# Kernel tuning notes

Measured on AMD Instinct MI355X. Metric: run time of the kernel, lower is better.

The kernel has to match this reference:

```python
import jax, jax.numpy as jnp
import numpy as np
from jax import lax

K = 3            # exact neighbors per node in setup -> inner loop bound
MAX_STEPS = K + 1  # each step removes a candidate; sentinel ends the loop


def setup_inputs() -> dict:
    key = jax.random.key(0)
    ks = jax.random.split(key, 10)
    N, Fin, E, H1, H2 = 128, 512, 128, 256, 128
    nbrs = jax.random.randint(ks[0], (N, K), 0, N)
    adj = jnp.zeros((N, N), jnp.float32).at[jnp.arange(N)[:, None], nbrs].set(1.0)
    feature_origin = jax.random.normal(ks[1], (N, Fin), jnp.float32)
    labels = jax.random.randint(ks[2], (N,), 0, 7)

    def lin(k, fi, fo):
        return (jax.random.normal(k, (fi, fo), jnp.float32) / np.float32(np.sqrt(fi)))

    return {
        "adj": adj, "feature_origin": feature_origin, "labels": labels,
        "W_e": lin(ks[3], Fin, E), "b_e": jnp.zeros((E,), jnp.float32),
        "W1": lin(ks[4], 2 * E, H1), "b1": jnp.zeros((H1,), jnp.float32),
        "W2": lin(ks[5], H1, H2), "b2": jnp.zeros((H2,), jnp.float32),
        "w_lk": lin(ks[6], H2, 1), "b_lk": jnp.zeros((1,), jnp.float32),
        "w_act": lin(ks[7], H2, 2), "b_act": jnp.zeros((2,), jnp.float32),
    }


def _forward(adj, feature_origin, W_e, b_e, W1, b1, W2, b2, w_lk, b_lk, w_act, b_act):
    N = feature_origin.shape[0]
    E = W_e.shape[1]
    embed = lambda x: jax.nn.relu(x @ W_e + b_e)
    mlp = lambda s: jax.nn.relu(jax.nn.relu(s @ W1 + b1) @ W2 + b2)
    feature0 = embed(feature_origin)                      # [N, E]
    # original quirk: `if v > 0` -> node 0 (and sentinel) get a zero neighbor feature
    nonzero_row = (jnp.arange(N) > 0)[:, None]

    def node_fn(carry, i):
        feature, updated = carry
        cand = adj[i] != 0                                # remaining candidate mask
        sel = jnp.zeros((N,), bool)                       # signal_neighbor_i as mask

        def step_fn(st, _):
            feature, cand, sel, updated, done = st
            x_i = feature[i]
            nbr = jnp.where(nonzero_row, feature, 0.0)
            s = jnp.concatenate([jnp.broadcast_to(x_i, (N, E)), nbr], axis=-1)
            sentinel = jnp.concatenate([x_i, jnp.zeros_like(x_i)])[None]
            s = jnp.concatenate([s, sentinel], axis=0)    # [N+1, 2E]
            hidden = mlp(s)                               # [N+1, H2]
            lk = (hidden @ w_lk + b_lk)[:, 0]             # [N+1]
            valid = jnp.concatenate([cand, jnp.ones((1,), bool)])
            # deterministic surrogate for Categorical sampling: argmax of dist
            ut = jnp.argmax(jnp.where(valid, lk, -jnp.inf))
            is_end = ut == N
            skip = done | is_end
            utc = jnp.minimum(ut, N - 1)
            at = (jnp.argmax(hidden[utc] @ w_act + b_act) == 1).astype(feature.dtype)
            x_ut = feature_origin[utc]
            x_self = feature_origin[i]
            self_f = sel.astype(feature.dtype)
            cnt = self_f.sum()
            sel_sum = self_f @ feature_origin
            hv = (sel_sum + at * x_ut + x_self) / (cnt + at + 1.0)
            feat2 = feature.at[i].set(embed(hv)).at[utc].set(embed(x_ut))
            feature = jnp.where(skip, feature, feat2)
            upd2 = updated.at[i].set(True).at[utc].set(True)
            updated = jnp.where(skip, updated, upd2)
            sel = sel.at[utc].set(jnp.where(skip, sel[utc], (at == 1.0) | sel[utc]))
            cand = cand.at[utc].set(jnp.where(skip, cand[utc], False))
            return (feature, cand, sel, updated, skip), None

        (feature, _, _, updated, _), _ = lax.scan(
            step_fn, (feature, cand, sel, updated, jnp.array(False)),
            None, length=MAX_STEPS)
        return (feature, updated), None

    (feature, updated), _ = lax.scan(
        node_fn, (feature0, jnp.zeros((N,), bool)), jnp.arange(N))
    # embedding mirrors every write to feature; untouched rows stay zero
    return jnp.where(updated[:, None], feature, 0.0)


def reference(adj, feature_origin, labels, W_e, b_e, W1, b1, W2, b2, w_lk, b_lk, w_act, b_act):
    return _forward(adj, feature_origin, W_e, b_e, W1, b1, W2, b2,
                    w_lk, b_lk, w_act, b_act)
```

## Files before the change

kernel.cpp:

```cpp
#include <hip/hip_runtime.h>
#include <math.h>

constexpr int Nn  = 128;
constexpr int FIN = 512;
constexpr int EE  = 128;
constexpr int H1n = 256;
constexpr int H2n = 128;

__global__ void precomp1(const float* __restrict__ fo, const float* __restrict__ We,
                         const float* __restrict__ be,
                         float* __restrict__ G0, float* __restrict__ feat)
{
    const int n = blockIdx.x;
    const int j = threadIdx.x;
    float acc = 0.f;
    for (int k = 0; k < FIN; ++k)
        acc += fo[n * FIN + k] * We[k * EE + j];
    G0[n * EE + j] = acc;
    feat[n * EE + j] = fmaxf(acc + be[j], 0.f);
}

__global__ void precomp2(const float* __restrict__ G0, const float* __restrict__ be,
                         const float* __restrict__ W1,
                         float* __restrict__ Bcur, float* __restrict__ B0)
{
    __shared__ float f[EE];
    const int n = blockIdx.x;
    const int j = threadIdx.x;
    if (j < EE) f[j] = fmaxf(G0[n * EE + j] + be[j], 0.f);
    __syncthreads();
    float acc = 0.f;
    for (int k = 0; k < EE; ++k)
        acc += f[k] * W1[(EE + k) * H1n + j];
    Bcur[n * H1n + j] = acc;
    if (B0) B0[n * H1n + j] = acc;
}

__global__ __launch_bounds__(512, 2) void seqk(
    const float* __restrict__ adj,  const float* __restrict__ W1,
    const float* __restrict__ b1,   const float* __restrict__ W2,
    const float* __restrict__ b2,   const float* __restrict__ wlk,
    const float* __restrict__ blkb, const float* __restrict__ wact,
    const float* __restrict__ bact, const float* __restrict__ be,
    const float* __restrict__ G0,   const float* __restrict__ B0,
    float* __restrict__ feat,       float* __restrict__ Bcur)
{
    __shared__ float w2t[H2n * H1n];
    __shared__ float x[EE];
    __shared__ float u[H1n];
    __shared__ float ubi[H1n];
    __shared__ float h1[4][H1n];
    __shared__ float h2[4][H2n];
    __shared__ float pa[4][4][H2n];
    __shared__ float gsum[EE], rowf[EE], sbe[EE];
    __shared__ float sb1[H1n], sb2[H2n], swlk[H2n], swact[2 * H2n];
    __shared__ float rb_lk[8], rb_a0[8], rb_a1[8];
    __shared__ float sblk, sba0, sba1;
    __shared__ int   candlist[4];
    __shared__ unsigned long long cand_mask[2], sel_mask[2], upd_mask[2];
    __shared__ int   ncand_s, ut_s, at_s, brk_s, rr_s, needb_s, xdirty_s;
    __shared__ float cnt_s;

    const int tid = threadIdx.x;

    float w1reg[128];
    {
        const int col = tid & 255;
        const int rbase = (tid < 256) ? 0 : EE;
        #pragma unroll
        for (int k = 0; k < 128; ++k)
            w1reg[k] = W1[(rbase + k) * H1n + col];
    }
    for (int idx = tid; idx < H1n * H2n; idx += 512) {
        const int k = idx >> 7, j = idx & 127;
        const int cg = k >> 2, w = k & 3;
        w2t[j * H1n + (((cg ^ (j & 7)) << 2) | w)] = W2[k * H2n + j];
    }
    if (tid < EE)  sbe[tid] = be[tid];
    if (tid < H1n) sb1[tid] = b1[tid];
    if (tid < H2n) { sb2[tid] = b2[tid]; swlk[tid] = wlk[tid]; }
    if (tid < 2 * H2n) swact[tid] = wact[tid];
    if (tid == 0) { sblk = blkb[0]; sba0 = bact[0]; sba1 = bact[1]; }
    if (tid < 2) upd_mask[tid] = 0ULL;
    __syncthreads();

    for (int i = 0; i < Nn; ++i) {
        if (tid < EE) { gsum[tid] = 0.f; x[tid] = feat[i * EE + tid]; }
        if (tid == 0) { cnt_s = 0.f; sel_mask[0] = 0ULL; sel_mask[1] = 0ULL; xdirty_s = 0; }
        if (tid < Nn) {
            const bool c = adj[i * Nn + tid] != 0.f;
            const unsigned long long m = __ballot(c);
            if ((tid & 63) == 0) cand_mask[tid >> 6] = m;
        }
        __syncthreads();
        if (tid == 0) {
            int nc = 0, selfc = 0;
            for (int w = 0; w < 2; ++w) {
                unsigned long long m = cand_mask[w];
                while (m && nc < 4) {
                    const int b = __builtin_ctzll(m);
                    const int v = w * 64 + b;
                    candlist[nc++] = v;
                    if (v == i) selfc = 1;
                    m &= m - 1;
                }
            }
            ncand_s = nc; needb_s = selfc;
        }
        __syncthreads();

        for (int s = 0; s < 4; ++s) {
            if (tid < 256 || needb_s) {
                float a0 = 0.f, a1 = 0.f, a2 = 0.f, a3 = 0.f;
                #pragma unroll
                for (int q = 0; q < 32; ++q) {
                    const float4 xv = *reinterpret_cast<const float4*>(&x[q * 4]);
                    a0 += xv.x * w1reg[q * 4 + 0];
                    a1 += xv.y * w1reg[q * 4 + 1];
                    a2 += xv.z * w1reg[q * 4 + 2];
                    a3 += xv.w * w1reg[q * 4 + 3];
                }
                const float sres = (a0 + a1) + (a2 + a3);
                if (tid < 256) u[tid] = sres; else ubi[tid - 256] = sres;
            }
            __syncthreads();

            {
                const int nrows = ncand_s + 1;
                #pragma unroll
                for (int hh = 0; hh < 2; ++hh) {
                    const int idx = hh * 512 + tid;
                    const int r = idx >> 8, k = idx & 255;
                    float hv = 0.f;
                    if (r < nrows) {
                        const int v = (r < ncand_s) ? candlist[r] : -1;
                        float Bv = 0.f;
                        if (v > 0) Bv = (v == i && needb_s) ? ubi[k] : Bcur[v * H1n + k];
                        hv = fmaxf(u[k] + Bv + sb1[k], 0.f);
                    }
                    h1[r][k] = hv;
                }
            }
            __syncthreads();

            {
                const int kq = tid >> 7, j = tid & 127;
                const int sw = j & 7;
                float ac0 = 0.f, ac1 = 0.f, ac2 = 0.f, ac3 = 0.f;
                #pragma unroll
                for (int kk = 0; kk < 16; ++kk) {
                    const int cg = kq * 16 + kk;
                    const float4 wv = *reinterpret_cast<const float4*>(
                        &w2t[j * H1n + ((cg ^ sw) << 2)]);
                    const int k0 = cg << 2;
                    const float4 h0 = *reinterpret_cast<const float4*>(&h1[0][k0]);
                    const float4 h1v = *reinterpret_cast<const float4*>(&h1[1][k0]);
                    const float4 h2v = *reinterpret_cast<const float4*>(&h1[2][k0]);
                    const float4 h3v = *reinterpret_cast<const float4*>(&h1[3][k0]);
                    ac0 += h0.x * wv.x + h0.y * wv.y + h0.z * wv.z + h0.w * wv.w;
                    ac1 += h1v.x * wv.x + h1v.y * wv.y + h1v.z * wv.z + h1v.w * wv.w;
                    ac2 += h2v.x * wv.x + h2v.y * wv.y + h2v.z * wv.z + h2v.w * wv.w;
                    ac3 += h3v.x * wv.x + h3v.y * wv.y + h3v.z * wv.z + h3v.w * wv.w;
                }
                pa[kq][0][j] = ac0; pa[kq][1][j] = ac1;
                pa[kq][2][j] = ac2; pa[kq][3][j] = ac3;
            }
            __syncthreads();

            {
                const int r = tid >> 7, j = tid & 127;
                const float v = pa[0][r][j] + pa[1][r][j] + pa[2][r][j] + pa[3][r][j]
                                + sb2[j];
                const float hval = fmaxf(v, 0.f);
                h2[r][j] = hval;
                float plk = hval * swlk[j];
                float p0  = hval * swact[2 * j];
                float p1  = hval * swact[2 * j + 1];
                #pragma unroll
                for (int off = 32; off; off >>= 1) {
                    plk += __shfl_down(plk, off);
                    p0  += __shfl_down(p0, off);
                    p1  += __shfl_down(p1, off);
                }
                if ((tid & 63) == 0) {
                    const int w = tid >> 6;
                    rb_lk[w] = plk; rb_a0[w] = p0; rb_a1[w] = p1;
                }
            }
            __syncthreads();

            if (tid == 0) {
                float lkv[4];
                #pragma unroll
                for (int r = 0; r < 4; ++r) lkv[r] = rb_lk[2 * r] + rb_lk[2 * r + 1] + sblk;
                float bv = -INFINITY; int ut = -1, rsel = -1;
                for (int r2 = 0; r2 < ncand_s; ++r2)
                    if (lkv[r2] > bv) { bv = lkv[r2]; ut = candlist[r2]; rsel = r2; }
                if (ut < 0 || lkv[ncand_s] > bv) ut = Nn;
                ut_s = ut;
                brk_s = (ut == Nn);
                if (!brk_s) {
                    rr_s = rsel;
                    const float a0 = rb_a0[2 * rsel] + rb_a0[2 * rsel + 1] + sba0;
                    const float a1 = rb_a1[2 * rsel] + rb_a1[2 * rsel + 1] + sba1;
                    at_s = (a1 > a0) ? 1 : 0;
                }
            }
            __syncthreads();
            if (brk_s) break;

            {
                const int utc = ut_s;
                const float at = (float)at_s;
                const bool selOld = (sel_mask[utc >> 6] >> (utc & 63)) & 1ULL;
                const float denom = cnt_s + at + 1.0f;
                if (tid < EE) {
                    const float g_ut = G0[utc * EE + tid];
                    const float futc = fmaxf(g_ut + sbe[tid], 0.f);
                    const float z = (gsum[tid] + at * g_ut + G0[i * EE + tid]) / denom
                                    + sbe[tid];
                    float nx = fmaxf(z, 0.f);
                    if (utc == i) nx = futc;
                    x[tid] = nx;
                    if (utc != i) feat[i * EE + tid] = nx;
                    feat[utc * EE + tid] = futc;
                    rowf[tid] = futc;
                    if (at_s && !selOld) gsum[tid] += g_ut;
                }
                if (B0 != nullptr && tid < H1n)
                    Bcur[utc * H1n + tid] = B0[utc * H1n + tid];
            }
            __syncthreads();

            if (tid == 0) {
                const int utc = ut_s;
                const bool selOld = (sel_mask[utc >> 6] >> (utc & 63)) & 1ULL;
                if (at_s && !selOld) { cnt_s += 1.f; sel_mask[utc >> 6] |= (1ULL << (utc & 63)); }
                cand_mask[utc >> 6] &= ~(1ULL << (utc & 63));
                upd_mask[i >> 6]   |= (1ULL << (i & 63));
                upd_mask[utc >> 6] |= (1ULL << (utc & 63));
                xdirty_s = (utc != i) ? 1 : 0;
                int nc = 0, selfc = 0;
                for (int w = 0; w < 2; ++w) {
                    unsigned long long m = cand_mask[w];
                    while (m && nc < 4) {
                        const int b = __builtin_ctzll(m);
                        const int v = w * 64 + b;
                        candlist[nc++] = v;
                        if (v == i) selfc = 1;
                        m &= m - 1;
                    }
                }
                ncand_s = nc; needb_s = selfc;
            }
            if (B0 == nullptr && tid >= 256) {
                float a0 = 0.f, a1 = 0.f, a2 = 0.f, a3 = 0.f;
                #pragma unroll
                for (int q = 0; q < 32; ++q) {
                    const float4 xv = *reinterpret_cast<const float4*>(&rowf[q * 4]);
                    a0 += xv.x * w1reg[q * 4 + 0];
                    a1 += xv.y * w1reg[q * 4 + 1];
                    a2 += xv.z * w1reg[q * 4 + 2];
                    a3 += xv.w * w1reg[q * 4 + 3];
                }
                Bcur[ut_s * H1n + (tid - 256)] = (a0 + a1) + (a2 + a3);
            }
            __syncthreads();
        }

        if (xdirty_s && tid >= 256) {
            float a0 = 0.f, a1 = 0.f, a2 = 0.f, a3 = 0.f;
            #pragma unroll
            for (int q = 0; q < 32; ++q) {
                const float4 xv = *reinterpret_cast<const float4*>(&x[q * 4]);
                a0 += xv.x * w1reg[q * 4 + 0];
                a1 += xv.y * w1reg[q * 4 + 1];
                a2 += xv.z * w1reg[q * 4 + 2];
                a3 += xv.w * w1reg[q * 4 + 3];
            }
            Bcur[i * H1n + (tid - 256)] = (a0 + a1) + (a2 + a3);
        }
        __syncthreads();
    }

    for (int idx = tid; idx < Nn * EE; idx += 512) {
        const int n = idx >> 7;
        const float v = feat[idx];
        feat[idx] = ((upd_mask[n >> 6] >> (n & 63)) & 1ULL) ? v : 0.f;
    }
}

extern "C" void kernel_launch(void* const* d_in, const int* in_sizes, int n_in,
                              void* d_out, int out_size, void* d_ws, size_t ws_size,
                              hipStream_t stream)
{
    (void)in_sizes; (void)n_in; (void)out_size;
    const float* adj  = (const float*)d_in[0];
    const float* fo   = (const float*)d_in[1];
    const float* We   = (const float*)d_in[3];
    const float* be   = (const float*)d_in[4];
    const float* W1   = (const float*)d_in[5];
    const float* b1   = (const float*)d_in[6];
    const float* W2   = (const float*)d_in[7];
    const float* b2   = (const float*)d_in[8];
    const float* wlk  = (const float*)d_in[9];
    const float* blkb = (const float*)d_in[10];
    const float* wact = (const float*)d_in[11];
    const float* bact = (const float*)d_in[12];

    float* ws   = (float*)d_ws;
    float* G0   = ws;
    float* Bcur = ws + 16384;
    float* B0   = (ws_size >= (size_t)(64 + 128 + 128) * 1024) ? (ws + 49152) : nullptr;
    float* feat = (float*)d_out;

    hipLaunchKernelGGL(precomp1, dim3(Nn), dim3(EE), 0, stream, fo, We, be, G0, feat);
    hipLaunchKernelGGL(precomp2, dim3(Nn), dim3(H1n), 0, stream, G0, be, W1, Bcur, B0);
    hipLaunchKernelGGL(seqk, dim3(1), dim3(512), 0, stream,
                       adj, W1, b1, W2, b2, wlk, blkb, wact, bact, be,
                       G0, B0, feat, Bcur);
}
```

Measured before the change: 1.970 ms.

## Move per-step control to registers, keep Bcur in LDS and W2 in registers

Result: slower. 2.285 ms (+16.0%).

```diff
diff --git a/kernel.cpp b/kernel.cpp
--- a/kernel.cpp
+++ b/kernel.cpp
@@ -22,7 +22,7 @@
 
 __global__ void precomp2(const float* __restrict__ G0, const float* __restrict__ be,
                          const float* __restrict__ W1,
-                         float* __restrict__ Bcur, float* __restrict__ B0)
+                         float* __restrict__ BcurG)
 {
     __shared__ float f[EE];
     const int n = blockIdx.x;
@@ -32,8 +32,7 @@
     float acc = 0.f;
     for (int k = 0; k < EE; ++k)
         acc += f[k] * W1[(EE + k) * H1n + j];
-    Bcur[n * H1n + j] = acc;
-    if (B0) B0[n * H1n + j] = acc;
+    BcurG[n * H1n + j] = acc;
 }
 
 __global__ __launch_bounds__(512, 2) void seqk(
@@ -42,24 +41,19 @@
     const float* __restrict__ b2,   const float* __restrict__ wlk,
     const float* __restrict__ blkb, const float* __restrict__ wact,
     const float* __restrict__ bact, const float* __restrict__ be,
-    const float* __restrict__ G0,   const float* __restrict__ B0,
-    float* __restrict__ feat,       float* __restrict__ Bcur)
+    const float* __restrict__ G0,   const float* __restrict__ BcurG,
+    float* __restrict__ feat)
 {
-    __shared__ float w2t[H2n * H1n];
-    __shared__ float x[EE];
+    __shared__ float bc[Nn * H1n];
+    __shared__ float h1[4][H1n];
+    __shared__ float pa[4][4][H2n];
     __shared__ float u[H1n];
     __shared__ float ubi[H1n];
-    __shared__ float h1[4][H1n];
-    __shared__ float h2[4][H2n];
-    __shared__ float pa[4][4][H2n];
-    __shared__ float gsum[EE], rowf[EE], sbe[EE];
-    __shared__ float sb1[H1n], sb2[H2n], swlk[H2n], swact[2 * H2n];
+    __shared__ float xsh[EE], gi[EE], gsum[EE];
+    __shared__ float gc[3 * EE];
+    __shared__ float sbe[EE], sb1[H1n], sb2[H2n], swlk[H2n], swact[2 * H2n];
     __shared__ float rb_lk[8], rb_a0[8], rb_a1[8];
-    __shared__ float sblk, sba0, sba1;
-    __shared__ int   candlist[4];
-    __shared__ unsigned long long cand_mask[2], sel_mask[2], upd_mask[2];
-    __shared__ int   ncand_s, ut_s, at_s, brk_s, rr_s, needb_s, xdirty_s;
-    __shared__ float cnt_s;
+    __shared__ unsigned long long mlds[2];
 
     const int tid = threadIdx.x;
 
@@ -71,50 +65,70 @@
         for (int k = 0; k < 128; ++k)
             w1reg[k] = W1[(rbase + k) * H1n + col];
     }
-    for (int idx = tid; idx < H1n * H2n; idx += 512) {
-        const int k = idx >> 7, j = idx & 127;
-        const int cg = k >> 2, w = k & 3;
-        w2t[j * H1n + (((cg ^ (j & 7)) << 2) | w)] = W2[k * H2n + j];
+    float w2reg[64];
+    {
+        const int kq = tid >> 7, j = tid & 127;
+        #pragma unroll
+        for (int kk = 0; kk < 64; ++kk)
+            w2reg[kk] = W2[(kq * 64 + kk) * H2n + j];
+    }
+    #pragma unroll
+    for (int q = 0; q < 16; ++q) {
+        const int idx = (q * 512 + tid) * 4;
+        *reinterpret_cast<float4*>(&bc[idx]) =
+            *reinterpret_cast<const float4*>(&BcurG[idx]);
     }
     if (tid < EE)  sbe[tid] = be[tid];
     if (tid < H1n) sb1[tid] = b1[tid];
     if (tid < H2n) { sb2[tid] = b2[tid]; swlk[tid] = wlk[tid]; }
     if (tid < 2 * H2n) swact[tid] = wact[tid];
-    if (tid == 0) { sblk = blkb[0]; sba0 = bact[0]; sba1 = bact[1]; }
-    if (tid < 2) upd_mask[tid] = 0ULL;
+    const float r_blk = blkb[0], r_ba0 = bact[0], r_ba1 = bact[1];
+    unsigned long long um0 = 0ULL, um1 = 0ULL;
     __syncthreads();
 
     for (int i = 0; i < Nn; ++i) {
-        if (tid < EE) { gsum[tid] = 0.f; x[tid] = feat[i * EE + tid]; }
-        if (tid == 0) { cnt_s = 0.f; sel_mask[0] = 0ULL; sel_mask[1] = 0ULL; xdirty_s = 0; }
+        if (tid < EE) { xsh[tid] = feat[i * EE + tid]; gsum[tid] = 0.f; }
+        if (tid < 32)
+            *reinterpret_cast<float4*>(&gi[tid * 4]) =
+                *reinterpret_cast<const float4*>(&G0[i * EE + tid * 4]);
         if (tid < Nn) {
             const bool c = adj[i * Nn + tid] != 0.f;
             const unsigned long long m = __ballot(c);
-            if ((tid & 63) == 0) cand_mask[tid >> 6] = m;
+            if ((tid & 63) == 0) mlds[tid >> 6] = m;
         }
         __syncthreads();
-        if (tid == 0) {
-            int nc = 0, selfc = 0;
-            for (int w = 0; w < 2; ++w) {
-                unsigned long long m = cand_mask[w];
-                while (m && nc < 4) {
-                    const int b = __builtin_ctzll(m);
-                    const int v = w * 64 + b;
-                    candlist[nc++] = v;
-                    if (v == i) selfc = 1;
-                    m &= m - 1;
-                }
-            }
-            ncand_s = nc; needb_s = selfc;
-        }
-        __syncthreads();
+        unsigned long long cm0 = mlds[0], cm1 = mlds[1];
+        unsigned long long sel0 = 0ULL, sel1 = 0ULL;
+        float cnt = 0.f;
+        int xdirty = 0;
 
         for (int s = 0; s < 4; ++s) {
-            if (tid < 256 || needb_s) {
+            int cl[4]; int ncand = 0;
+            {
+                unsigned long long m0 = cm0, m1 = cm1;
+                #pragma unroll
+                for (int t = 0; t < 4; ++t) {
+                    int v = -1;
+                    if (m0) { v = __builtin_ctzll(m0); m0 &= m0 - 1; }
+                    else if (m1) { v = 64 + __builtin_ctzll(m1); m1 &= m1 - 1; }
+                    cl[t] = v;
+                    if (v >= 0) ++ncand;
+                }
+            }
+            const int needb = (cl[0] == i) | (cl[1] == i) | (cl[2] == i) | (cl[3] == i);
+
+            const int pr = tid >> 5, pf = tid & 31;
+            const bool havegc = (tid < 96) && (pr < ncand);
+            float4 gtmp;
+            if (havegc) {
+                const int v = (pr == 0) ? cl[0] : (pr == 1) ? cl[1] : cl[2];
+                gtmp = *reinterpret_cast<const float4*>(&G0[v * EE + pf * 4]);
+            }
+            if (tid < 256 || needb) {
                 float a0 = 0.f, a1 = 0.f, a2 = 0.f, a3 = 0.f;
                 #pragma unroll
                 for (int q = 0; q < 32; ++q) {
-                    const float4 xv = *reinterpret_cast<const float4*>(&x[q * 4]);
+                    const float4 xv = *reinterpret_cast<const float4*>(&xsh[q * 4]);
                     a0 += xv.x * w1reg[q * 4 + 0];
                     a1 += xv.y * w1reg[q * 4 + 1];
                     a2 += xv.z * w1reg[q * 4 + 2];
@@ -123,19 +137,22 @@
                 const float sres = (a0 + a1) + (a2 + a3);
                 if (tid < 256) u[tid] = sres; else ubi[tid - 256] = sres;
             }
+            if (havegc)
+                *reinterpret_cast<float4*>(&gc[pr * EE + pf * 4]) = gtmp;
             __syncthreads();
 
             {
-                const int nrows = ncand_s + 1;
+                const int half = tid >> 8, k = tid & 255;
                 #pragma unroll
                 for (int hh = 0; hh < 2; ++hh) {
-                    const int idx = hh * 512 + tid;
-                    const int r = idx >> 8, k = idx & 255;
+                    const int r = hh * 2 + half;
+                    const int v = (half == 0) ? (hh == 0 ? cl[0] : cl[2])
+                                              : (hh == 0 ? cl[1] : cl[3]);
                     float hv = 0.f;
-                    if (r < nrows) {
-                        const int v = (r < ncand_s) ? candlist[r] : -1;
+                    if (r <= ncand) {
                         float Bv = 0.f;
-                        if (v > 0) Bv = (v == i && needb_s) ? ubi[k] : Bcur[v * H1n + k];
+                        if (r < ncand && v > 0)
+                            Bv = (v == i && needb) ? ubi[k] : bc[v * H1n + k];
                         hv = fmaxf(u[k] + Bv + sb1[k], 0.f);
                     }
                     h1[r][k] = hv;
@@ -145,22 +162,20 @@
 
             {
                 const int kq = tid >> 7, j = tid & 127;
-                const int sw = j & 7;
+                const int kb = kq * 64;
                 float ac0 = 0.f, ac1 = 0.f, ac2 = 0.f, ac3 = 0.f;
                 #pragma unroll
-                for (int kk = 0; kk < 16; ++kk) {
-                    const int cg = kq * 16 + kk;
-                    const float4 wv = *reinterpret_cast<const float4*>(
-                        &w2t[j * H1n + ((cg ^ sw) << 2)]);
-                    const int k0 = cg << 2;
-                    const float4 h0 = *reinterpret_cast<const float4*>(&h1[0][k0]);
-                    const float4 h1v = *reinterpret_cast<const float4*>(&h1[1][k0]);
-                    const float4 h2v = *reinterpret_cast<const float4*>(&h1[2][k0]);
-                    const float4 h3v = *reinterpret_cast<const float4*>(&h1[3][k0]);
-                    ac0 += h0.x * wv.x + h0.y * wv.y + h0.z * wv.z + h0.w * wv.w;
-                    ac1 += h1v.x * wv.x + h1v.y * wv.y + h1v.z * wv.z + h1v.w * wv.w;
-                    ac2 += h2v.x * wv.x + h2v.y * wv.y + h2v.z * wv.z + h2v.w * wv.w;
-                    ac3 += h3v.x * wv.x + h3v.y * wv.y + h3v.z * wv.z + h3v.w * wv.w;
+                for (int kk = 0; kk < 64; kk += 4) {
+                    const float4 h0 = *reinterpret_cast<const float4*>(&h1[0][kb + kk]);
+                    const float4 hv1 = *reinterpret_cast<const float4*>(&h1[1][kb + kk]);
+                    const float4 hv2 = *reinterpret_cast<const float4*>(&h1[2][kb + kk]);
+                    const float4 hv3 = *reinterpret_cast<const float4*>(&h1[3][kb + kk]);
+                    const float w0 = w2reg[kk], w1_ = w2reg[kk + 1];
+                    const float w2_ = w2reg[kk + 2], w3 = w2reg[kk + 3];
+                    ac0 += h0.x * w0 + h0.y * w1_ + h0.z * w2_ + h0.w * w3;
+                    ac1 += hv1.x * w0 + hv1.y * w1_ + hv1.z * w2_ + hv1.w * w3;
+                    ac2 += hv2.x * w0 + hv2.y * w1_ + hv2.z * w2_ + hv2.w * w3;
+                    ac3 += hv3.x * w0 + hv3.y * w1_ + hv3.z * w2_ + hv3.w * w3;
                 }
                 pa[kq][0][j] = ac0; pa[kq][1][j] = ac1;
                 pa[kq][2][j] = ac2; pa[kq][3][j] = ac3;
@@ -172,7 +187,6 @@
                 const float v = pa[0][r][j] + pa[1][r][j] + pa[2][r][j] + pa[3][r][j]
                                 + sb2[j];
                 const float hval = fmaxf(v, 0.f);
-                h2[r][j] = hval;
                 float plk = hval * swlk[j];
                 float p0  = hval * swact[2 * j];
                 float p1  = hval * swact[2 * j + 1];
@@ -189,104 +203,79 @@
             }
             __syncthreads();
 
-            if (tid == 0) {
-                float lkv[4];
-                #pragma unroll
-                for (int r = 0; r < 4; ++r) lkv[r] = rb_lk[2 * r] + rb_lk[2 * r + 1] + sblk;
-                float bv = -INFINITY; int ut = -1, rsel = -1;
-                for (int r2 = 0; r2 < ncand_s; ++r2)
-                    if (lkv[r2] > bv) { bv = lkv[r2]; ut = candlist[r2]; rsel = r2; }
-                if (ut < 0 || lkv[ncand_s] > bv) ut = Nn;
-                ut_s = ut;
-                brk_s = (ut == Nn);
-                if (!brk_s) {
-                    rr_s = rsel;
-                    const float a0 = rb_a0[2 * rsel] + rb_a0[2 * rsel + 1] + sba0;
-                    const float a1 = rb_a1[2 * rsel] + rb_a1[2 * rsel + 1] + sba1;
-                    at_s = (a1 > a0) ? 1 : 0;
-                }
-            }
-            __syncthreads();
-            if (brk_s) break;
-
-            {
-                const int utc = ut_s;
-                const float at = (float)at_s;
-                const bool selOld = (sel_mask[utc >> 6] >> (utc & 63)) & 1ULL;
-                const float denom = cnt_s + at + 1.0f;
-                if (tid < EE) {
-                    const float g_ut = G0[utc * EE + tid];
-                    const float futc = fmaxf(g_ut + sbe[tid], 0.f);
-                    const float z = (gsum[tid] + at * g_ut + G0[i * EE + tid]) / denom
-                                    + sbe[tid];
-                    float nx = fmaxf(z, 0.f);
-                    if (utc == i) nx = futc;
-                    x[tid] = nx;
-                    if (utc != i) feat[i * EE + tid] = nx;
-                    feat[utc * EE + tid] = futc;
-                    rowf[tid] = futc;
-                    if (at_s && !selOld) gsum[tid] += g_ut;
-                }
-                if (B0 != nullptr && tid < H1n)
-                    Bcur[utc * H1n + tid] = B0[utc * H1n + tid];
-            }
-            __syncthreads();
-
-            if (tid == 0) {
-                const int utc = ut_s;
-                const bool selOld = (sel_mask[utc >> 6] >> (utc & 63)) & 1ULL;
-                if (at_s && !selOld) { cnt_s += 1.f; sel_mask[utc >> 6] |= (1ULL << (utc & 63)); }
-                cand_mask[utc >> 6] &= ~(1ULL << (utc & 63));
-                upd_mask[i >> 6]   |= (1ULL << (i & 63));
-                upd_mask[utc >> 6] |= (1ULL << (utc & 63));
-                xdirty_s = (utc != i) ? 1 : 0;
-                int nc = 0, selfc = 0;
-                for (int w = 0; w < 2; ++w) {
-                    unsigned long long m = cand_mask[w];
-                    while (m && nc < 4) {
-                        const int b = __builtin_ctzll(m);
-                        const int v = w * 64 + b;
-                        candlist[nc++] = v;
-                        if (v == i) selfc = 1;
-                        m &= m - 1;
-                    }
-                }
-                ncand_s = nc; needb_s = selfc;
-            }
-            if (B0 == nullptr && tid >= 256) {
-                float a0 = 0.f, a1 = 0.f, a2 = 0.f, a3 = 0.f;
-                #pragma unroll
-                for (int q = 0; q < 32; ++q) {
-                    const float4 xv = *reinterpret_cast<const float4*>(&rowf[q * 4]);
-                    a0 += xv.x * w1reg[q * 4 + 0];
-                    a1 += xv.y * w1reg[q * 4 + 1];
-                    a2 += xv.z * w1reg[q * 4 + 2];
-                    a3 += xv.w * w1reg[q * 4 + 3];
-                }
-                Bcur[ut_s * H1n + (tid - 256)] = (a0 + a1) + (a2 + a3);
+            float lkv[4];
+            #pragma unroll
+            for (int r = 0; r < 4; ++r)
+                lkv[r] = rb_lk[2 * r] + rb_lk[2 * r + 1] + r_blk;
+            float bv = -INFINITY; int ut = -1, rsel = -1;
+            #pragma unroll
+            for (int r = 0; r < 4; ++r)
+                if (r < ncand && lkv[r] > bv) { bv = lkv[r]; ut = cl[r]; rsel = r; }
+            const float slk = (ncand == 0) ? lkv[0] : (ncand == 1) ? lkv[1]
+                            : (ncand == 2) ? lkv[2] : lkv[3];
+            const bool brk = (ut < 0) || (slk > bv);
+            if (brk) break;
+            const float a0v = rb_a0[2 * rsel] + rb_a0[2 * rsel + 1] + r_ba0;
+            const float a1v = rb_a1[2 * rsel] + rb_a1[2 * rsel + 1] + r_ba1;
+            const int at = (a1v > a0v) ? 1 : 0;
+            const int utc = ut;
+            const bool selOld =
+                ((utc < 64 ? (sel0 >> utc) : (sel1 >> (utc - 64))) & 1ULL) != 0ULL;
+            const float denom = cnt + (float)at + 1.0f;
+            if (at && !selOld) {
+                cnt += 1.f;
+                if (utc < 64) sel0 |= 1ULL << utc; else sel1 |= 1ULL << (utc - 64);
+            }
+            if (utc < 64) cm0 &= ~(1ULL << utc); else cm1 &= ~(1ULL << (utc - 64));
+            if (i < 64) um0 |= 1ULL << i; else um1 |= 1ULL << (i - 64);
+            if (utc < 64) um0 |= 1ULL << utc; else um1 |= 1ULL << (utc - 64);
+            xdirty = (utc != i) ? 1 : 0;
+
+            if (tid < EE) {
+                const float g_ut = gc[rsel * EE + tid];
+                const float futc = fmaxf(g_ut + sbe[tid], 0.f);
+                const float z = (gsum[tid] + (float)at * g_ut + gi[tid]) / denom
+                                + sbe[tid];
+                float nx = fmaxf(z, 0.f);
+                if (utc == i) nx = futc;
+                xsh[tid] = nx;
+                if (utc != i) feat[i * EE + tid] = nx;
+                feat[utc * EE + tid] = futc;
+                if (at && !selOld) gsum[tid] += g_ut;
+            } else if (tid >= 256) {
+                const int c = tid - 256;
+                float acc = 0.f;
+                #pragma unroll
+                for (int k = 0; k < 128; ++k) {
+                    const float f = fmaxf(gc[rsel * EE + k] + sbe[k], 0.f);
+                    acc = fmaf(f, w1reg[k], acc);
+                }
+                bc[utc * H1n + c] = acc;
             }
             __syncthreads();
         }
 
-        if (xdirty_s && tid >= 256) {
+        if (xdirty && tid >= 256) {
+            const int c = tid - 256;
             float a0 = 0.f, a1 = 0.f, a2 = 0.f, a3 = 0.f;
             #pragma unroll
             for (int q = 0; q < 32; ++q) {
-                const float4 xv = *reinterpret_cast<const float4*>(&x[q * 4]);
+                const float4 xv = *reinterpret_cast<const float4*>(&xsh[q * 4]);
                 a0 += xv.x * w1reg[q * 4 + 0];
                 a1 += xv.y * w1reg[q * 4 + 1];
                 a2 += xv.z * w1reg[q * 4 + 2];
                 a3 += xv.w * w1reg[q * 4 + 3];
             }
-            Bcur[i * H1n + (tid - 256)] = (a0 + a1) + (a2 + a3);
+            bc[i * H1n + c] = (a0 + a1) + (a2 + a3);
         }
         __syncthreads();
     }
 
     for (int idx = tid; idx < Nn * EE; idx += 512) {
         const int n = idx >> 7;
+        const bool upd = ((n < 64 ? (um0 >> n) : (um1 >> (n - 64))) & 1ULL) != 0ULL;
         const float v = feat[idx];
-        feat[idx] = ((upd_mask[n >> 6] >> (n & 63)) & 1ULL) ? v : 0.f;
+        feat[idx] = upd ? v : 0.f;
     }
 }
 
@@ -294,7 +283,7 @@
                               void* d_out, int out_size, void* d_ws, size_t ws_size,
                               hipStream_t stream)
 {
-    (void)in_sizes; (void)n_in; (void)out_size;
+    (void)in_sizes; (void)n_in; (void)out_size; (void)ws_size;
     const float* adj  = (const float*)d_in[0];
     const float* fo   = (const float*)d_in[1];
     const float* We   = (const float*)d_in[3];
@@ -308,15 +297,14 @@
     const float* wact = (const float*)d_in[11];
     const float* bact = (const float*)d_in[12];
 
-    float* ws   = (float*)d_ws;
-    float* G0   = ws;
-    float* Bcur = ws + 16384;
-    float* B0   = (ws_size >= (size_t)(64 + 128 + 128) * 1024) ? (ws + 49152) : nullptr;
-    float* feat = (float*)d_out;
+    float* ws    = (float*)d_ws;
+    float* G0    = ws;
+    float* BcurG = ws + 16384;
+    float* feat  = (float*)d_out;
 
     hipLaunchKernelGGL(precomp1, dim3(Nn), dim3(EE), 0, stream, fo, We, be, G0, feat);
-    hipLaunchKernelGGL(precomp2, dim3(Nn), dim3(H1n), 0, stream, G0, be, W1, Bcur, B0);
+    hipLaunchKernelGGL(precomp2, dim3(Nn), dim3(H1n), 0, stream, G0, be, W1, BcurG);
     hipLaunchKernelGGL(seqk, dim3(1), dim3(512), 0, stream,
                        adj, W1, b1, W2, b2, wlk, blkb, wact, bact, be,
-                       G0, B0, feat, Bcur);
+                       G0, BcurG, feat);
 }
```
